# Kernel tuning notes

Measured on AMD Instinct MI355X. Metric: run time of the kernel, lower is better.

The kernel has to match this reference:

```python
import jax, jax.numpy as jnp
import numpy as np

N, E, F_IN, HID, C = 100000, 3200000, 512, 16, 40


def setup_inputs() -> dict:
    key = jax.random.key(0)
    k1, k2, k3, k4 = jax.random.split(key, 4)
    x = jax.random.normal(k1, (N, F_IN), dtype=jnp.float32)
    edge_index = jax.random.randint(k2, (2, E), 0, N, dtype=jnp.int64)
    W1 = jax.random.normal(k3, (F_IN, HID), dtype=jnp.float32) * (1.0 / np.sqrt(F_IN))
    b1 = jnp.zeros((HID,), dtype=jnp.float32)
    W2 = jax.random.normal(k4, (HID, C), dtype=jnp.float32) * (1.0 / np.sqrt(HID))
    b2 = jnp.zeros((C,), dtype=jnp.float32)
    return {"x": x, "edge_index": edge_index, "W1": W1, "b1": b1, "W2": W2, "b2": b2}


def reference(x, edge_index, W1, b1, W2, b2):
    n = x.shape[0]
    # PyG GCNConv: add self-loops, symmetric normalization D^-1/2 (A+I) D^-1/2
    loops = jnp.arange(n, dtype=edge_index.dtype)
    row = jnp.concatenate([edge_index[0], loops])  # source nodes
    col = jnp.concatenate([edge_index[1], loops])  # target nodes
    ones = jnp.ones(row.shape[0], dtype=x.dtype)
    deg = jax.ops.segment_sum(ones, col, num_segments=n)
    dinv = jnp.where(deg > 0, jax.lax.rsqrt(deg), 0.0).astype(x.dtype)
    norm = dinv[row] * dinv[col]  # [E+N]

    def gcn_conv(h, W, b):
        h = h @ W                                   # linear transform first (small out dim)
        msg = h[row] * norm[:, None]                # gather + scale
        agg = jax.ops.segment_sum(msg, col, num_segments=n)  # scatter-add
        return agg + b

    h = jax.nn.relu(gcn_conv(x, W1, b1))
    # dropout is identity in eval mode (F.dropout(training=self.training))
    out = gcn_conv(h, W2, b2)
    return jax.nn.log_softmax(out, axis=1)
```

## Files before the change

### kernel.cpp

```cpp
#include <hip/hip_runtime.h>
#include <hip/hip_fp16.h>

#define F_IN 512
#define HID  16
#define NCLS 40
#define KSPL 4
#define KH   (F_IN / KSPL)
#define BSH2 8
#define BNODES 256
#define NBMAX 512
#define EPB 8192
#define CAP 12288

__device__ __forceinline__ float4 ld_h4(const __half* p) {
    uint2 u = *reinterpret_cast<const uint2*>(p);
    __half2 a = *reinterpret_cast<__half2*>(&u.x);
    __half2 b = *reinterpret_cast<__half2*>(&u.y);
    float2 fa = __half22float2(a), fb = __half22float2(b);
    return make_float4(fa.x, fa.y, fb.x, fb.y);
}

__device__ __forceinline__ void st_h4(__half* p, float4 v) {
    __half2 a = __floats2half2_rn(v.x, v.y);
    __half2 b = __floats2half2_rn(v.z, v.w);
    uint2 u;
    u.x = *reinterpret_cast<unsigned*>(&a);
    u.y = *reinterpret_cast<unsigned*>(&b);
    *reinterpret_cast<uint2*>(p) = u;
}

__global__ __launch_bounds__(512) void k_front(
    const int* __restrict__ col, int* __restrict__ lhists,
    const float* __restrict__ x, const float* __restrict__ W1,
    __half* __restrict__ yp4, int ne, int n, int neb, int gblk) {
    __shared__ int lh[NBMAX];
    int t = threadIdx.x;
    if (blockIdx.x < neb) {
        lh[t] = 0;
        __syncthreads();
        int base = blockIdx.x * EPB;
        int end = min(ne, base + EPB);
        int e = base + t * 4;
        for (; e + 3 < end; e += 2048) {
            int4 c = *reinterpret_cast<const int4*>(col + e);
            atomicAdd(&lh[c.x >> BSH2], 1);
            atomicAdd(&lh[c.y >> BSH2], 1);
            atomicAdd(&lh[c.z >> BSH2], 1);
            atomicAdd(&lh[c.w >> BSH2], 1);
        }
        for (; e < end; ++e) atomicAdd(&lh[col[e] >> BSH2], 1);
        __syncthreads();
        lhists[(size_t)blockIdx.x * NBMAX + t] = lh[t];
        return;
    }
    int fb = blockIdx.x - neb;
    int part = fb / gblk;
    int node = (fb % gblk) * 512 + t;
    if (node >= n) return;
    const float* xr = x + (size_t)node * F_IN + part * KH;
    const float* Wb = W1 + (size_t)part * KH * HID;
    float acc[HID];
#pragma unroll
    for (int j = 0; j < HID; ++j) acc[j] = 0.f;
#define STEP(av, kk) \
    _Pragma("unroll") for (int j = 0; j < HID; ++j) acc[j] = fmaf(av, w[(kk) * HID + j], acc[j]);
#pragma unroll
    for (int k = 0; k < KH; k += 16) {
        const float4* xv = reinterpret_cast<const float4*>(xr + k);
        float4 a0 = xv[0], a1 = xv[1], a2 = xv[2], a3 = xv[3];
        const float* w = Wb + (size_t)k * HID;
        STEP(a0.x, 0)  STEP(a0.y, 1)  STEP(a0.z, 2)  STEP(a0.w, 3)
        STEP(a1.x, 4)  STEP(a1.y, 5)  STEP(a1.z, 6)  STEP(a1.w, 7)
        STEP(a2.x, 8)  STEP(a2.y, 9)  STEP(a2.z, 10) STEP(a2.w, 11)
        STEP(a3.x, 12) STEP(a3.y, 13) STEP(a3.z, 14) STEP(a3.w, 15)
    }
    __half* o = yp4 + ((size_t)part * n + node) * HID;
#pragma unroll
    for (int q = 0; q < 4; ++q)
        st_h4(o + q * 4, make_float4(acc[4 * q], acc[4 * q + 1], acc[4 * q + 2], acc[4 * q + 3]));
}

__global__ __launch_bounds__(512) void k_bscan(
    const int* __restrict__ lhists, int* __restrict__ bstart,
    int* __restrict__ bcur, int nb, int neb) {
    __shared__ int sh[512];
    int t = threadIdx.x;
    int s = 0;
#pragma unroll 4
    for (int j = 0; j < neb; ++j) s += lhists[(size_t)j * NBMAX + t];
    int v = (t < nb) ? s : 0;
    sh[t] = v;
    __syncthreads();
    for (int off = 1; off < 512; off <<= 1) {
        int u = (t >= off) ? sh[t - off] : 0;
        __syncthreads();
        sh[t] += u;
        __syncthreads();
    }
    if (t < nb) {
        int ex = sh[t] - v;
        bstart[t] = ex;
        bcur[t] = ex;
    }
    if (t == nb - 1) bstart[nb] = sh[t];
}

__global__ __launch_bounds__(512) void k_bucket(
    const int* __restrict__ row, const int* __restrict__ col,
    const int* __restrict__ lhists, int* __restrict__ bcur,
    int* __restrict__ packed, int ne) {
    __shared__ int lbase[NBMAX];
    __shared__ int gbase[NBMAX];
    __shared__ int lcur[NBMAX];
    __shared__ int buf[EPB];
    __shared__ unsigned short bof[EPB];
    int t = threadIdx.x;
    int own = lhists[(size_t)blockIdx.x * NBMAX + t];
    lcur[t] = 0;
    if (own > 0) gbase[t] = atomicAdd(&bcur[t], own);
    lbase[t] = own;
    __syncthreads();
    for (int off = 1; off < 512; off <<= 1) {
        int v = (t >= off) ? lbase[t - off] : 0;
        __syncthreads();
        lbase[t] += v;
        __syncthreads();
    }
    int ex = lbase[t] - own;
    __syncthreads();
    lbase[t] = ex;
    __syncthreads();
    int base = blockIdx.x * EPB;
    int end = min(ne, base + EPB);
    for (int e = base + t; e < end; e += 512) {
        int r = row[e], c = col[e];
        int gb = c >> BSH2;
        int rk = atomicAdd(&lcur[gb], 1);
        int pos = lbase[gb] + rk;
        buf[pos] = r | ((c & (BNODES - 1)) << 24);
        bof[pos] = (unsigned short)gb;
    }
    __syncthreads();
    int m = end - base;
    for (int k = t; k < m; k += 512) {
        int gb = bof[k];
        packed[gbase[gb] + (k - lbase[gb])] = buf[k];
    }
}

__global__ __launch_bounds__(512) void k_csr(
    int* __restrict__ cnt, const int* __restrict__ bstart,
    const int* __restrict__ packed, int* __restrict__ ptr,
    int* __restrict__ rows_sorted, int n, int nb) {
    __shared__ int sh[BNODES];
    __shared__ int lcur[BNODES];
    __shared__ int lrows[CAP];
    int b = blockIdx.x, t = threadIdx.x;
    int c0 = b << BSH2;
    int nloc = min(BNODES, n - c0);
    int s = bstart[b], e = bstart[b + 1];
    int m = e - s;
    if (t < BNODES) sh[t] = 0;
    __syncthreads();
    for (int k = t; k < m; k += 512)
        atomicAdd(&sh[((unsigned)packed[s + k]) >> 24], 1);
    __syncthreads();
    int own = (t < BNODES) ? sh[t] : 0;
    if (t < nloc) cnt[c0 + t] = own;
    for (int off = 1; off < BNODES; off <<= 1) {
        int v = (t >= off && t < BNODES) ? sh[t - off] : 0;
        __syncthreads();
        if (t < BNODES) sh[t] += v;
        __syncthreads();
    }
    if (t < nloc) {
        int ex = sh[t] - own;
        ptr[c0 + t] = s + ex;
        lcur[t] = ex;
    }
    if (b == nb - 1 && t == 0) ptr[n] = e;
    __syncthreads();
    if (m <= CAP) {
        for (int k = t; k < m; k += 512) {
            int p = packed[s + k];
            int pos = atomicAdd(&lcur[((unsigned)p) >> 24], 1);
            lrows[pos] = p & 0xFFFFFF;
        }
        __syncthreads();
        for (int k = t; k < m; k += 512) rows_sorted[s + k] = lrows[k];
    } else {
        for (int k = t; k < m; k += 512) {
            int p = packed[s + k];
            int pos = atomicAdd(&lcur[((unsigned)p) >> 24], 1);
            rows_sorted[s + pos] = p & 0xFFFFFF;
        }
    }
}

__global__ void k_comb(const __half* __restrict__ yp4, const int* __restrict__ cnt,
                       __half* __restrict__ yp, int n) {
    int i = blockIdx.x * blockDim.x + threadIdx.x;
    if (i >= n * 4) return;
    int node = i >> 2;
    float di = rsqrtf((float)(cnt[node] + 1));
    size_t S = (size_t)n * HID;
    float sx = 0.f, sy = 0.f, sz = 0.f, sw = 0.f;
#pragma unroll
    for (int s = 0; s < KSPL; ++s) {
        float4 a = ld_h4(yp4 + s * S + (size_t)i * 4);
        sx += a.x; sy += a.y; sz += a.z; sw += a.w;
    }
    st_h4(yp + (size_t)i * 4, make_float4(di * sx, di * sy, di * sz, di * sw));
}

template <bool RELU>
__global__ void k_agg(const int* __restrict__ ptr, const int* __restrict__ rows_sorted,
                      const __half* __restrict__ src, const int* __restrict__ cnt,
                      const float* __restrict__ b1,
                      __half* __restrict__ dst_h, float* __restrict__ dst_f, int n) {
    int t = blockIdx.x * blockDim.x + threadIdx.x;
    int g = t >> 2;
    if (g >= n) return;
    int q = (t & 3) << 2;
    float4 acc = ld_h4(src + (size_t)g * HID + q);
    int s = ptr[g], e2 = ptr[g + 1];
    int k = s;
    for (; k + 3 < e2; k += 4) {
        int r0 = rows_sorted[k],     r1 = rows_sorted[k + 1];
        int r2 = rows_sorted[k + 2], r3 = rows_sorted[k + 3];
        float4 v0 = ld_h4(src + (size_t)r0 * HID + q);
        float4 v1 = ld_h4(src + (size_t)r1 * HID + q);
        float4 v2 = ld_h4(src + (size_t)r2 * HID + q);
        float4 v3 = ld_h4(src + (size_t)r3 * HID + q);
        acc.x += (v0.x + v1.x) + (v2.x + v3.x);
        acc.y += (v0.y + v1.y) + (v2.y + v3.y);
        acc.z += (v0.z + v1.z) + (v2.z + v3.z);
        acc.w += (v0.w + v1.w) + (v2.w + v3.w);
    }
    for (; k < e2; ++k) {
        int r0 = rows_sorted[k];
        float4 v0 = ld_h4(src + (size_t)r0 * HID + q);
        acc.x += v0.x; acc.y += v0.y; acc.z += v0.z; acc.w += v0.w;
    }
    float d = rsqrtf((float)(cnt[g] + 1));
    if (RELU) {
        float4 bb = *reinterpret_cast<const float4*>(b1 + q);
        float4 o;
        o.x = d * fmaxf(fmaf(d, acc.x, bb.x), 0.f);
        o.y = d * fmaxf(fmaf(d, acc.y, bb.y), 0.f);
        o.z = d * fmaxf(fmaf(d, acc.z, bb.z), 0.f);
        o.w = d * fmaxf(fmaf(d, acc.w, bb.w), 0.f);
        st_h4(dst_h + (size_t)g * HID + q, o);
    } else {
        float4 o = make_float4(d * acc.x, d * acc.y, d * acc.z, d * acc.w);
        *reinterpret_cast<float4*>(dst_f + (size_t)g * HID + q) = o;
    }
}

__global__ void k_final(const float* __restrict__ agg2, const float* __restrict__ W2,
                        const float* __restrict__ b2, float* __restrict__ out, int n) {
    int node = blockIdx.x * blockDim.x + threadIdx.x;
    if (node >= n) return;
    const float4* ar = reinterpret_cast<const float4*>(agg2 + (size_t)node * HID);
    float a[HID];
#pragma unroll
    for (int q = 0; q < 4; ++q) {
        float4 t = ar[q];
        a[4 * q] = t.x; a[4 * q + 1] = t.y; a[4 * q + 2] = t.z; a[4 * q + 3] = t.w;
    }
    float z[NCLS];
#pragma unroll
    for (int j = 0; j < NCLS; ++j) z[j] = b2[j];
#pragma unroll
    for (int i = 0; i < HID; ++i) {
        const float* w = W2 + (size_t)i * NCLS;
        float ai = a[i];
#pragma unroll
        for (int j = 0; j < NCLS; ++j) z[j] = fmaf(ai, w[j], z[j]);
    }
    float m = z[0];
#pragma unroll
    for (int j = 1; j < NCLS; ++j) m = fmaxf(m, z[j]);
    float s = 0.f;
#pragma unroll
    for (int j = 0; j < NCLS; ++j) s += __expf(z[j] - m);
    float ls = m + __logf(s);
    float* o = out + (size_t)node * NCLS;
#pragma unroll
    for (int q = 0; q < NCLS / 4; ++q)
        *reinterpret_cast<float4*>(o + 4 * q) =
            make_float4(z[4 * q] - ls, z[4 * q + 1] - ls, z[4 * q + 2] - ls, z[4 * q + 3] - ls);
}

extern "C" void kernel_launch(void* const* d_in, const int* in_sizes, int n_in,
                              void* d_out, int out_size, void* d_ws, size_t ws_size,
                              hipStream_t stream) {
    const float* x  = (const float*)d_in[0];
    const int*   ei = (const int*)d_in[1];
    const float* W1 = (const float*)d_in[2];
    const float* b1 = (const float*)d_in[3];
    const float* W2 = (const float*)d_in[4];
    const float* b2 = (const float*)d_in[5];
    float* out = (float*)d_out;

    const int N = in_sizes[0] / F_IN;
    const int E = in_sizes[1] / 2;
    const int* row = ei;
    const int* col = ei + E;
    const int NBUCK = (N + BNODES - 1) >> BSH2;
    const int NEB = (E + EPB - 1) / EPB;
    const int GBLK = (N + 511) >> 9;

    char* w = (char*)d_ws;
    int*   cnt    = (int*)w;   w += (size_t)N * 4;
    int*   bstart = (int*)w;   w += (size_t)(NBMAX + 1) * 4;
    int*   bcur   = (int*)w;   w += (size_t)NBMAX * 4;
    int*   lhists = (int*)w;   w += (size_t)NEB * NBMAX * 4;
    int*   ptr    = (int*)w;   w += (size_t)(N + 1) * 4;
    int*   rows_sorted = (int*)w; w += (size_t)E * 4;
    int*   packed = (int*)w;   w += (size_t)E * 4;
    __half* yp4   = (__half*)w; w += (size_t)KSPL * N * HID * 2;
    __half* yp_h  = (__half*)w; w += (size_t)N * HID * 2;
    __half* hp_h  = (__half*)w; w += (size_t)N * HID * 2;
    float* agg2   = (float*)w; w += (size_t)N * HID * 4;

    const int B = 256;
    k_front <<<NEB + KSPL * GBLK, 512, 0, stream>>>(col, lhists, x, W1, yp4, E, N, NEB, GBLK);
    k_bscan <<<1, 512, 0, stream>>>(lhists, bstart, bcur, NBUCK, NEB);
    k_bucket<<<NEB, 512, 0, stream>>>(row, col, lhists, bcur, packed, E);
    k_csr   <<<NBUCK, 512, 0, stream>>>(cnt, bstart, packed, ptr, rows_sorted, N, NBUCK);
    k_comb  <<<((N * 4) + B - 1) / B, B, 0, stream>>>(yp4, cnt, yp_h, N);
    k_agg<true> <<<((N * 4) + B - 1) / B, B, 0, stream>>>(ptr, rows_sorted, yp_h, cnt, b1, hp_h, nullptr, N);
    k_agg<false><<<((N * 4) + B - 1) / B, B, 0, stream>>>(ptr, rows_sorted, hp_h, cnt, nullptr, nullptr, agg2, N);
    k_final <<<(N + B - 1) / B, B, 0, stream>>>(agg2, W2, b2, out, N);
}
```

Before: 226.4 us.

## Reduce K-split partial sums in shared memory inside the first-layer GEMM

Moves the four K-split partial products for each node into one block and reduces them in LDS before a single fp16 store. This removes the fp16 partial buffer and its separate combine kernel, leaving only a normalisation-scale pass. That saves several MB of global writes and reads. In exchange it adds a large shared-memory array per block and a block barrier, and changes the thread-to-node mapping for the x reads.

```diff
diff --git a/kernel.cpp b/kernel.cpp
--- a/kernel.cpp
+++ b/kernel.cpp
@@ -6,6 +6,8 @@
 #define NCLS 40
 #define KSPL 4
 #define KH   (F_IN / KSPL)
+#define GNOD 128
+#define RSTR 68
 #define BSH2 8
 #define BNODES 256
 #define NBMAX 512
@@ -32,10 +34,11 @@
 __global__ __launch_bounds__(512) void k_front(
     const int* __restrict__ col, int* __restrict__ lhists,
     const float* __restrict__ x, const float* __restrict__ W1,
-    __half* __restrict__ yp4, int ne, int n, int neb, int gblk) {
-    __shared__ int lh[NBMAX];
+    __half* __restrict__ yp, int ne, int n, int neb) {
+    __shared__ float red[GNOD * RSTR];
     int t = threadIdx.x;
     if (blockIdx.x < neb) {
+        int* lh = (int*)red;
         lh[t] = 0;
         __syncthreads();
         int base = blockIdx.x * EPB;
@@ -54,30 +57,42 @@
         return;
     }
     int fb = blockIdx.x - neb;
-    int part = fb / gblk;
-    int node = (fb % gblk) * 512 + t;
-    if (node >= n) return;
-    const float* xr = x + (size_t)node * F_IN + part * KH;
-    const float* Wb = W1 + (size_t)part * KH * HID;
+    int nl = t >> 2;
+    int part = t & 3;
+    int node = fb * GNOD + nl;
+    bool alive = node < n;
     float acc[HID];
 #pragma unroll
     for (int j = 0; j < HID; ++j) acc[j] = 0.f;
+    if (alive) {
+        const float* xr = x + (size_t)node * F_IN + part * KH;
+        const float* Wb = W1 + (size_t)part * KH * HID;
 #define STEP(av, kk) \
     _Pragma("unroll") for (int j = 0; j < HID; ++j) acc[j] = fmaf(av, w[(kk) * HID + j], acc[j]);
 #pragma unroll
-    for (int k = 0; k < KH; k += 16) {
-        const float4* xv = reinterpret_cast<const float4*>(xr + k);
-        float4 a0 = xv[0], a1 = xv[1], a2 = xv[2], a3 = xv[3];
-        const float* w = Wb + (size_t)k * HID;
-        STEP(a0.x, 0)  STEP(a0.y, 1)  STEP(a0.z, 2)  STEP(a0.w, 3)
-        STEP(a1.x, 4)  STEP(a1.y, 5)  STEP(a1.z, 6)  STEP(a1.w, 7)
-        STEP(a2.x, 8)  STEP(a2.y, 9)  STEP(a2.z, 10) STEP(a2.w, 11)
-        STEP(a3.x, 12) STEP(a3.y, 13) STEP(a3.z, 14) STEP(a3.w, 15)
-    }
-    __half* o = yp4 + ((size_t)part * n + node) * HID;
-#pragma unroll
-    for (int q = 0; q < 4; ++q)
-        st_h4(o + q * 4, make_float4(acc[4 * q], acc[4 * q + 1], acc[4 * q + 2], acc[4 * q + 3]));
+        for (int k = 0; k < KH; k += 16) {
+            const float4* xv = reinterpret_cast<const float4*>(xr + k);
+            float4 a0 = xv[0], a1 = xv[1], a2 = xv[2], a3 = xv[3];
+            const float* w = Wb + (size_t)k * HID;
+            STEP(a0.x, 0)  STEP(a0.y, 1)  STEP(a0.z, 2)  STEP(a0.w, 3)
+            STEP(a1.x, 4)  STEP(a1.y, 5)  STEP(a1.z, 6)  STEP(a1.w, 7)
+            STEP(a2.x, 8)  STEP(a2.y, 9)  STEP(a2.z, 10) STEP(a2.w, 11)
+            STEP(a3.x, 12) STEP(a3.y, 13) STEP(a3.z, 14) STEP(a3.w, 15)
+        }
+    }
+    float* r = red + nl * RSTR + part * HID;
+#pragma unroll
+    for (int j = 0; j < HID; ++j) r[j] = acc[j];
+    __syncthreads();
+    if (alive) {
+        int q = part << 2;
+        const float* rb = red + nl * RSTR;
+        float s0 = rb[q]     + rb[HID + q]     + rb[2 * HID + q]     + rb[3 * HID + q];
+        float s1 = rb[q + 1] + rb[HID + q + 1] + rb[2 * HID + q + 1] + rb[3 * HID + q + 1];
+        float s2 = rb[q + 2] + rb[HID + q + 2] + rb[2 * HID + q + 2] + rb[3 * HID + q + 2];
+        float s3 = rb[q + 3] + rb[HID + q + 3] + rb[2 * HID + q + 3] + rb[3 * HID + q + 3];
+        st_h4(yp + (size_t)node * HID + q, make_float4(s0, s1, s2, s3));
+    }
 }
 
 __global__ __launch_bounds__(512) void k_bscan(
@@ -197,20 +212,13 @@
     }
 }
 
-__global__ void k_comb(const __half* __restrict__ yp4, const int* __restrict__ cnt,
-                       __half* __restrict__ yp, int n) {
+__global__ void k_scale(__half* __restrict__ yp, const int* __restrict__ cnt, int n) {
     int i = blockIdx.x * blockDim.x + threadIdx.x;
     if (i >= n * 4) return;
     int node = i >> 2;
     float di = rsqrtf((float)(cnt[node] + 1));
-    size_t S = (size_t)n * HID;
-    float sx = 0.f, sy = 0.f, sz = 0.f, sw = 0.f;
-#pragma unroll
-    for (int s = 0; s < KSPL; ++s) {
-        float4 a = ld_h4(yp4 + s * S + (size_t)i * 4);
-        sx += a.x; sy += a.y; sz += a.z; sw += a.w;
-    }
-    st_h4(yp + (size_t)i * 4, make_float4(di * sx, di * sy, di * sz, di * sw));
+    float4 a = ld_h4(yp + (size_t)i * 4);
+    st_h4(yp + (size_t)i * 4, make_float4(di * a.x, di * a.y, di * a.z, di * a.w));
 }
 
 template <bool RELU>
@@ -309,7 +317,7 @@
     const int* col = ei + E;
     const int NBUCK = (N + BNODES - 1) >> BSH2;
     const int NEB = (E + EPB - 1) / EPB;
-    const int GBLK = (N + 511) >> 9;
+    const int GB2 = (N + GNOD - 1) / GNOD;
 
     char* w = (char*)d_ws;
     int*   cnt    = (int*)w;   w += (size_t)N * 4;
@@ -319,17 +327,16 @@
     int*   ptr    = (int*)w;   w += (size_t)(N + 1) * 4;
     int*   rows_sorted = (int*)w; w += (size_t)E * 4;
     int*   packed = (int*)w;   w += (size_t)E * 4;
-    __half* yp4   = (__half*)w; w += (size_t)KSPL * N * HID * 2;
     __half* yp_h  = (__half*)w; w += (size_t)N * HID * 2;
     __half* hp_h  = (__half*)w; w += (size_t)N * HID * 2;
     float* agg2   = (float*)w; w += (size_t)N * HID * 4;
 
     const int B = 256;
-    k_front <<<NEB + KSPL * GBLK, 512, 0, stream>>>(col, lhists, x, W1, yp4, E, N, NEB, GBLK);
+    k_front <<<NEB + GB2, 512, 0, stream>>>(col, lhists, x, W1, yp_h, E, N, NEB);
     k_bscan <<<1, 512, 0, stream>>>(lhists, bstart, bcur, NBUCK, NEB);
     k_bucket<<<NEB, 512, 0, stream>>>(row, col, lhists, bcur, packed, E);
     k_csr   <<<NBUCK, 512, 0, stream>>>(cnt, bstart, packed, ptr, rows_sorted, N, NBUCK);
-    k_comb  <<<((N * 4) + B - 1) / B, B, 0, stream>>>(yp4, cnt, yp_h, N);
+    k_scale <<<((N * 4) + B - 1) / B, B, 0, stream>>>(yp_h, cnt, N);
     k_agg<true> <<<((N * 4) + B - 1) / B, B, 0, stream>>>(ptr, rows_sorted, yp_h, cnt, b1, hp_h, nullptr, N);
     k_agg<false><<<((N * 4) + B - 1) / B, B, 0, stream>>>(ptr, rows_sorted, hp_h, cnt, nullptr, nullptr, agg2, N);
     k_final <<<(N + B - 1) / B, B, 0, stream>>>(agg2, W2, b2, out, N);
```

New measurement: 633.3 us. 180% more time.
